# Optimization experiments

Measured on AMD Instinct MI355X. Metric: run time of the kernel, lower is better.

## Reference

```python
import jax, jax.numpy as jnp
import numpy as np

N = 50000   # nodes
E = 800000  # edges (avg degree 16)
DIMS = [(128, 128), (128, 128), (128, 64)]  # (in, out) per SAGEConv layer
EPS_BN = 1e-5
EPS_NORM = 1e-12


def _make_layer(key, din, dout):
    k1, k2 = jax.random.split(key)
    s = 1.0 / np.sqrt(din)
    return (
        jax.random.normal(k1, (dout, din), jnp.float32) * s,  # Wl: neighbor linear
        jnp.zeros((dout,), jnp.float32),                      # bl
        jax.random.normal(k2, (dout, din), jnp.float32) * s,  # Wr: root linear (no bias in PyG)
        jnp.ones((dout,), jnp.float32),                       # bn gamma
        jnp.zeros((dout,), jnp.float32),                      # bn beta
        jnp.zeros((dout,), jnp.float32),                      # bn running mean
        jnp.ones((dout,), jnp.float32),                       # bn running var
    )


def setup_inputs() -> dict:
    key = jax.random.key(0)
    kx, ke, k0, k1, k2 = jax.random.split(key, 5)
    inp = {
        "x": jax.random.normal(kx, (N, 128), jnp.float32),
        "edge_index": jax.random.randint(ke, (2, E), 0, N, dtype=jnp.int32),
    }
    for i, (k, (din, dout)) in enumerate(zip([k0, k1, k2], DIMS)):
        Wl, bl, Wr, g, b, rm, rv = _make_layer(k, din, dout)
        inp.update({f"Wl{i}": Wl, f"bl{i}": bl, f"Wr{i}": Wr,
                    f"g{i}": g, f"b{i}": b, f"rm{i}": rm, f"rv{i}": rv})
    return inp


def _sage_conv(x, src, dst, Wl, bl, Wr):
    # mean aggregation of incoming messages: gather src features, scatter-add at dst
    agg = jax.ops.segment_sum(x[src], dst, num_segments=N)          # [N, din]
    deg = jax.ops.segment_sum(jnp.ones((src.shape[0],), x.dtype), dst, num_segments=N)
    mean = agg / jnp.maximum(deg, 1.0)[:, None]
    return mean @ Wl.T + bl + x @ Wr.T


def _bn_eval(x, g, b, rm, rv):
    return g * (x - rm) * jax.lax.rsqrt(rv + EPS_BN) + b


def reference(x, edge_index,
              Wl0, bl0, Wr0, g0, b0, rm0, rv0,
              Wl1, bl1, Wr1, g1, b1, rm1, rv1,
              Wl2, bl2, Wr2, g2, b2, rm2, rv2):
    src, dst = edge_index[0], edge_index[1]
    layers = [
        (Wl0, bl0, Wr0, g0, b0, rm0, rv0),
        (Wl1, bl1, Wr1, g1, b1, rm1, rv1),
        (Wl2, bl2, Wr2, g2, b2, rm2, rv2),
    ]
    h = x
    for i, (Wl, bl, Wr, g, b, rm, rv) in enumerate(layers):
        h = _bn_eval(_sage_conv(h, src, dst, Wl, bl, Wr), g, b, rm, rv)
        if i < len(layers) - 1:
            h = jax.nn.relu(h)  # dropout is identity in eval mode
    # F.normalize(p=2, dim=1)
    return h / jnp.maximum(jnp.linalg.norm(h, axis=1, keepdims=True), EPS_NORM)
```

## Files before the change

### kernel.cpp

```cpp
#include <hip/hip_runtime.h>
#include <hip/hip_bf16.h>

#define CDIV(a,b) (((a)+(b)-1)/(b))
#define NBUCK_MAX 512
#define AGG_CAP  1536
#define AGGF_CAP 3072

typedef __attribute__((ext_vector_type(8))) short short8;
typedef __attribute__((ext_vector_type(4))) float f32x4;
typedef __attribute__((ext_vector_type(2))) float f32x2;

static __device__ __forceinline__ unsigned short f2bf(float f){
  union { float f; unsigned u; } v; v.f = f;
  unsigned r = v.u + 0x7fffu + ((v.u >> 16) & 1u);
  return (unsigned short)(r >> 16);
}
static __device__ __forceinline__ unsigned pack2(float lo, float hi){
  return (unsigned)f2bf(lo) | ((unsigned)f2bf(hi) << 16);
}
static __device__ __forceinline__ float bf2f(unsigned short s){
  union { unsigned u; float f; } v; v.u = ((unsigned)s) << 16; return v.f;
}
static __device__ __forceinline__ unsigned pk_fp8x4(float a, float b, float c, float d){
  int v = __builtin_amdgcn_cvt_pk_fp8_f32(a, b, 0, false);
  v = __builtin_amdgcn_cvt_pk_fp8_f32(c, d, v, true);
  return (unsigned)v;
}

#define ACCP16(v) { b0 += __builtin_amdgcn_cvt_pk_f32_fp8((int)v.x, false); \
                    b1 += __builtin_amdgcn_cvt_pk_f32_fp8((int)v.x, true);  \
                    b2 += __builtin_amdgcn_cvt_pk_f32_fp8((int)v.y, false); \
                    b3 += __builtin_amdgcn_cvt_pk_f32_fp8((int)v.y, true);  \
                    b4 += __builtin_amdgcn_cvt_pk_f32_fp8((int)v.z, false); \
                    b5 += __builtin_amdgcn_cvt_pk_f32_fp8((int)v.z, true);  \
                    b6 += __builtin_amdgcn_cvt_pk_f32_fp8((int)v.w, false); \
                    b7 += __builtin_amdgcn_cvt_pk_f32_fp8((int)v.w, true); }


struct WtpArgs {
  const float *W0, *W1, *bl, *g, *b, *rm, *rv;
  unsigned short* Bpk; float *sc; float *sh;
  int kblk, dout, do_bn, nblk, perm;
};

static __device__ __forceinline__ void wtp_one(const WtpArgs& a, int idx){
  int NB16 = a.kblk*32*a.dout;
  if (idx < NB16){
    int j = idx & 7, lane = (idx >> 3) & 63, rest = idx >> 9;
    int NT = a.dout >> 4;
    int nt = rest % NT, kk = rest / NT;
    int nn = nt*16 + (lane & 15);
    int k  = kk*32 + ((lane >> 4) * 8) + j;
    float v;
    if (k < 128){
      int kc = a.perm ? (((k & 7) << 4) | (k >> 3)) : k;
      v = a.W0[nn*128 + kc];
    } else {
      v = a.W1[nn*128 + (k - 128)];
    }
    a.Bpk[idx] = f2bf(v);
  } else if (a.do_bn && idx < NB16 + a.dout){
    int jj = idx - NB16;
    float s = a.g[jj] * rsqrtf(a.rv[jj] + 1e-5f);
    a.sc[jj] = s;
    a.sh[jj] = (a.bl[jj] - a.rm[jj]) * s + a.b[jj];
  }
}


__global__ __launch_bounds__(256) void k_prep(const float* __restrict__ x, int n4, unsigned* __restrict__ xb,
                                              unsigned* __restrict__ xq,
                                              const int* __restrict__ dst, int E,
                                              int* __restrict__ bcnt, int nbuck,
                                              int castBlocks, int histBlocks,
                                              WtpArgs a0, WtpArgs a1, WtpArgs a2, WtpArgs a3){
  __shared__ int s[NBUCK_MAX];
  int b = blockIdx.x, t = threadIdx.x;
  if (b < castBlocks){
    int i = b*256 + t;
    if (i < n4){
      float4 v = ((const float4*)x)[i];
      uint2 o; o.x = pack2(v.x, v.y); o.y = pack2(v.z, v.w);
      ((uint2*)xb)[i] = o;
      xq[i] = pk_fp8x4(v.x, v.y, v.z, v.w);
    }
    return;
  }
  b -= castBlocks;
  if (b < histBlocks){
    for (int i=t;i<nbuck;i+=256) s[i] = 0;
    __syncthreads();
    constexpr int EPT = 16;
    int e0 = b*256*EPT;
    #pragma unroll
    for (int i=0;i<EPT;i++){
      int e = e0 + i*256 + t;
      if (e < E) atomicAdd(&s[dst[e] >> 7], 1);
    }
    __syncthreads();
    for (int i=t;i<nbuck;i+=256){
      int c = s[i];
      if (c > 0) atomicAdd(&bcnt[i], c);
    }
    return;
  }
  b -= histBlocks;
  if (b < a0.nblk){ wtp_one(a0, b*256 + t); return; }
  b -= a0.nblk;
  if (b < a1.nblk){ wtp_one(a1, b*256 + t); return; }
  b -= a1.nblk;
  if (b < a2.nblk){ wtp_one(a2, b*256 + t); return; }
  b -= a2.nblk;
  wtp_one(a3, b*256 + t);
}

__global__ __launch_bounds__(256) void k_bucketA(const int* __restrict__ src, const int* __restrict__ dst,
                                                 int E, const int* __restrict__ bcnt,
                                                 int* __restrict__ bcur, unsigned* __restrict__ ebuf, int nbuck){
  __shared__ int scnt[NBUCK_MAX];
  __shared__ int sbase[NBUCK_MAX];
  __shared__ int sboff[NBUCK_MAX];
  __shared__ int ss[256];
  int t = threadIdx.x;
  {
    int a0 = (2*t   < nbuck) ? bcnt[2*t]   : 0;
    int a1 = (2*t+1 < nbuck) ? bcnt[2*t+1] : 0;
    ss[t] = a0 + a1; __syncthreads();
    for (int d=1; d<256; d<<=1){
      int u = (t>=d) ? ss[t-d] : 0;
      __syncthreads();
      ss[t] += u;
      __syncthreads();
    }
    int excl = ss[t] - (a0 + a1);
    if (2*t   < nbuck) sboff[2*t]   = excl;
    if (2*t+1 < nbuck) sboff[2*t+1] = excl + a0;
  }
  for (int i=t;i<nbuck;i+=256) scnt[i] = 0;
  __syncthreads();
  constexpr int EPT = 16;
  int e0 = blockIdx.x*256*EPT;
  int b[EPT]; unsigned pk[EPT];
  #pragma unroll
  for (int i=0;i<EPT;i++){
    int e = e0 + i*256 + t;
    if (e < E){
      int d = dst[e];
      b[i] = d >> 7;
      pk[i] = ((unsigned)(d & 127) << 16) | (unsigned)src[e];
      atomicAdd(&scnt[b[i]], 1);
    } else b[i] = -1;
  }
  __syncthreads();
  for (int i=t;i<nbuck;i+=256){
    int c = scnt[i];
    sbase[i] = (c > 0) ? atomicAdd(&bcur[i], c) : 0;
    scnt[i] = 0;
  }
  __syncthreads();
  #pragma unroll
  for (int i=0;i<EPT;i++){
    if (b[i] >= 0){
      int p = atomicAdd(&scnt[b[i]], 1);
      ebuf[(size_t)sboff[b[i]] + sbase[b[i]] + p] = pk[i];
    }
  }
}

__global__ __launch_bounds__(256) void k_bucketB(const unsigned* __restrict__ ebuf, const int* __restrict__ bcnt,
                                                 int nbuck, int E, int N,
                                                 int* __restrict__ offR, int* __restrict__ csr,
                                                 int* __restrict__ nodemap){
  __shared__ int sEx[NBUCK_MAX];
  __shared__ int ss[256];
  __shared__ int sdeg[128];
  __shared__ int sabs[129];
  __shared__ int cur[128];
  __shared__ unsigned skey[128];
  __shared__ int rof[128];
  int b = blockIdx.x, t = threadIdx.x;
  {
    int a0 = (2*t   < nbuck) ? bcnt[2*t]   : 0;
    int a1 = (2*t+1 < nbuck) ? bcnt[2*t+1] : 0;
    ss[t] = a0 + a1; __syncthreads();
    for (int d=1; d<256; d<<=1){
      int u = (t>=d) ? ss[t-d] : 0;
      __syncthreads();
      ss[t] += u;
      __syncthreads();
    }
    int excl = ss[t] - (a0 + a1);
    if (2*t   < nbuck) sEx[2*t]   = excl;
    if (2*t+1 < nbuck) sEx[2*t+1] = excl + a0;
  }
  if (t < 128){ sdeg[t] = 0; cur[t] = 0; }
  __syncthreads();
  int e0 = sEx[b];
  int e1 = (b+1 < nbuck) ? sEx[b+1] : E;
  for (int e = e0 + t; e < e1; e += 256)
    atomicAdd(&sdeg[ebuf[e] >> 16], 1);
  __syncthreads();
  if (t < 128) skey[t] = ((unsigned)sdeg[t] << 7) | (unsigned)(127 - t);
  __syncthreads();
  #pragma unroll
  for (int k=2; k<=128; k<<=1){
    #pragma unroll
    for (int j=k>>1; j>0; j>>=1){
      if (t < 128){
        int p = t ^ j;
        if (p > t){
          unsigned x = skey[t], y = skey[p];
          bool swap = ((t & k) == 0) ? (x < y) : (x > y);
          if (swap){ skey[t] = y; skey[p] = x; }
        }
      }
      __syncthreads();
    }
  }
  if (t < 128){
    int lid = 127 - (int)(skey[t] & 127u);
    rof[lid] = t;
    sdeg[t] = (int)(skey[t] >> 7);
  }
  __syncthreads();
  for (int d=1; d<128; d<<=1){
    int u = (t < 128 && t >= d) ? sdeg[t-d] : 0;
    __syncthreads();
    if (t < 128) sdeg[t] += u;
    __syncthreads();
  }
  if (t == 0) sabs[0] = e0;
  if (t < 128) sabs[t+1] = e0 + sdeg[t];
  __syncthreads();
  int n0 = b << 7, n1 = min(n0 + 128, N);
  int cnt = n1 - n0;
  if (t <= cnt) offR[n0 + t] = sabs[t];
  if (t < cnt)  nodemap[n0 + t] = n0 + (127 - (int)(skey[t] & 127u));
  for (int e = e0 + t; e < e1; e += 256){
    unsigned pr = ebuf[e];
    int ln = (int)(pr >> 16);
    int p = atomicAdd(&cur[ln], 1);
    csr[sabs[rof[ln]] + p] = (int)(pr & 0xffffu);
  }
}


__global__ __launch_bounds__(256) void k_agg(const uint4* __restrict__ hq4, const int* __restrict__ offR,
                                             const int* __restrict__ csr, const int* __restrict__ nodemap,
                                             int n, uint4* __restrict__ mean4){
  __shared__ int scsr[AGG_CAP];
  __shared__ int sw[2];
  int t = threadIdx.x;
  int nodeblk = blockIdx.x * 32;
  if (t < 2) sw[t] = offR[min(nodeblk + t*32, n)];
  __syncthreads();
  int e0b = sw[0];
  int span = sw[1] - e0b;
  for (int i = t; i < span && i < AGG_CAP; i += 256) scsr[i] = csr[e0b + i];
  __syncthreads();

  int lane = t & 63;
  int sl = lane & 7;
  int idx = nodeblk + (t >> 3);
  bool valid = idx < n;
  int s0 = valid ? offR[idx]   : 0;
  int s1 = valid ? offR[idx+1] : 0;
  int node = valid ? nodemap[idx] : 0;
  f32x2 b0={0,0},b1={0,0},b2={0,0},b3={0,0},b4={0,0},b5={0,0},b6={0,0},b7={0,0};
  int e = s0;
  for (; e + 8 <= s1; e += 8){
    int le = e - e0b;
    int i0,i1,i2,i3,i4,i5,i6,i7;
    if (le + 8 <= AGG_CAP){
      i0 = scsr[le];   i1 = scsr[le+1]; i2 = scsr[le+2]; i3 = scsr[le+3];
      i4 = scsr[le+4]; i5 = scsr[le+5]; i6 = scsr[le+6]; i7 = scsr[le+7];
    } else {
      i0 = csr[e];   i1 = csr[e+1]; i2 = csr[e+2]; i3 = csr[e+3];
      i4 = csr[e+4]; i5 = csr[e+5]; i6 = csr[e+6]; i7 = csr[e+7];
    }
    uint4 v0 = hq4[(size_t)i0*8 + sl];
    uint4 v1 = hq4[(size_t)i1*8 + sl];
    uint4 v2 = hq4[(size_t)i2*8 + sl];
    uint4 v3 = hq4[(size_t)i3*8 + sl];
    uint4 v4 = hq4[(size_t)i4*8 + sl];
    uint4 v5 = hq4[(size_t)i5*8 + sl];
    uint4 v6 = hq4[(size_t)i6*8 + sl];
    uint4 v7 = hq4[(size_t)i7*8 + sl];
    ACCP16(v0); ACCP16(v1); ACCP16(v2); ACCP16(v3);
    ACCP16(v4); ACCP16(v5); ACCP16(v6); ACCP16(v7);
  }
  for (; e + 4 <= s1; e += 4){
    int le = e - e0b;
    int i0,i1,i2,i3;
    if (le + 4 <= AGG_CAP){
      i0 = scsr[le]; i1 = scsr[le+1]; i2 = scsr[le+2]; i3 = scsr[le+3];
    } else {
      i0 = csr[e]; i1 = csr[e+1]; i2 = csr[e+2]; i3 = csr[e+3];
    }
    uint4 v0 = hq4[(size_t)i0*8 + sl];
    uint4 v1 = hq4[(size_t)i1*8 + sl];
    uint4 v2 = hq4[(size_t)i2*8 + sl];
    uint4 v3 = hq4[(size_t)i3*8 + sl];
    ACCP16(v0); ACCP16(v1); ACCP16(v2); ACCP16(v3);
  }
  for (; e < s1; e++){
    int le = e - e0b;
    int ii = (le < AGG_CAP) ? scsr[le] : csr[e];
    uint4 v = hq4[(size_t)ii*8 + sl];
    ACCP16(v);
  }
  if (valid){
    int d = s1 - s0;
    float inv = 1.0f / (float)(d > 0 ? d : 1);
    uint4 o0, o1;
    o0.x = pack2(b0.x*inv, b0.y*inv);  o0.y = pack2(b1.x*inv, b1.y*inv);
    o0.z = pack2(b2.x*inv, b2.y*inv);  o0.w = pack2(b3.x*inv, b3.y*inv);
    o1.x = pack2(b4.x*inv, b4.y*inv);  o1.y = pack2(b5.x*inv, b5.y*inv);
    o1.z = pack2(b6.x*inv, b6.y*inv);  o1.w = pack2(b7.x*inv, b7.y*inv);
    size_t base = (size_t)node*16 + (size_t)sl*2;
    mean4[base]   = o0;
    mean4[base+1] = o1;
  }
}


template<bool YL>
__global__ __launch_bounds__(256, 2) void k_gemm_hid(
    const unsigned short* __restrict__ A0, const unsigned short* __restrict__ A1,
    const unsigned short* __restrict__ Bpk, const float* __restrict__ sc,
    const float* __restrict__ sh, const unsigned short* __restrict__ BpkL,
    unsigned short* __restrict__ outh, unsigned* __restrict__ outq,
    unsigned* __restrict__ outyl, int n){
  __shared__ unsigned short Bs[256*128];
  int t = threadIdx.x;
  {
    const uint4* s = (const uint4*)Bpk;
    uint4* d = (uint4*)Bs;
    #pragma unroll
    for (int i=0;i<16;i++) d[i*256 + t] = s[i*256 + t];
  }
  __syncthreads();

  int lane = t & 63, w = t >> 6;
  int quad = lane >> 4, c = lane & 15;
  int mb = blockIdx.x*128, woff = w*32;
  int r0 = mb + woff + c;
  int r1 = r0 + 16;

  f32x4 acc[2][8];
  #pragma unroll
  for (int mt=0;mt<2;mt++)
    #pragma unroll
    for (int nt=0;nt<8;nt++) acc[mt][nt] = (f32x4){0.f,0.f,0.f,0.f};

  #pragma unroll
  for (int kk=0; kk<8; kk++){
    const unsigned short* ab = (kk >= 4) ? A1 : A0;
    int ka = (kk & 3)*32 + quad*8;
    short8 a0 = {0,0,0,0,0,0,0,0}, a1 = {0,0,0,0,0,0,0,0};
    if (r0 < n) a0 = *(const short8*)(ab + (size_t)r0*128 + ka);
    if (r1 < n) a1 = *(const short8*)(ab + (size_t)r1*128 + ka);
    #pragma unroll
    for (int nt=0; nt<8; nt++){
      short8 b = *(const short8*)&Bs[(size_t)((kk*8 + nt)*64 + lane)*8];
      acc[0][nt] = __builtin_amdgcn_mfma_f32_16x16x32_bf16(a0, b, acc[0][nt], 0, 0, 0);
      acc[1][nt] = __builtin_amdgcn_mfma_f32_16x16x32_bf16(a1, b, acc[1][nt], 0, 0, 0);
    }
  }

  float scv[8], shv[8];
  #pragma unroll
  for (int nt=0;nt<8;nt++){ scv[nt] = sc[nt*16 + c]; shv[nt] = sh[nt*16 + c]; }

  #pragma unroll
  for (int mt=0; mt<2; mt++){
    #pragma unroll
    for (int r=0;r<4;r++){
      int row = mb + woff + mt*16 + quad*4 + r;
      if (row < n){
        float u[8];
        #pragma unroll
        for (int nt=0;nt<8;nt++){
          float uu = acc[mt][nt][r]*scv[nt] + shv[nt];
          u[nt] = fmaxf(uu, 0.f);
          outh[(size_t)row*128 + nt*16 + c] = f2bf(u[nt]);
        }
        if constexpr (!YL){
          uint2 q;
          q.x = pk_fp8x4(u[0], u[1], u[2], u[3]);
          q.y = pk_fp8x4(u[4], u[5], u[6], u[7]);
          ((uint2*)outq)[(size_t)row*16 + c] = q;
        }
      }
    }
  }

  if constexpr (YL){
    __syncthreads();
    {
      uint4* d = (uint4*)Bs;
      const uint4* s4 = (const uint4*)outh;
      #pragma unroll
      for (int i=0;i<8;i++){
        int idx = i*256 + t;
        int row = idx >> 4;
        int gr = mb + row; if (gr > n-1) gr = n-1;
        d[idx] = s4[(size_t)gr*16 + (idx & 15)];
      }
      const uint4* sL = (const uint4*)BpkL;
      #pragma unroll
      for (int i=0;i<4;i++) d[2048 + i*256 + t] = sL[i*256 + t];
    }
    __syncthreads();
    f32x4 acc2[2][4];
    #pragma unroll
    for (int mt=0;mt<2;mt++)
      #pragma unroll
      for (int nt=0;nt<4;nt++) acc2[mt][nt] = (f32x4){0.f,0.f,0.f,0.f};
    int r0l = woff + c, r1l = r0l + 16;
    #pragma unroll
    for (int kk=0; kk<4; kk++){
      int ka = kk*32 + quad*8;
      short8 a0 = *(const short8*)&Bs[(size_t)r0l*128 + ka];
      short8 a1 = *(const short8*)&Bs[(size_t)r1l*128 + ka];
      #pragma unroll
      for (int nt=0; nt<4; nt++){
        short8 b = *(const short8*)&Bs[16384 + (size_t)((kk*4 + nt)*64 + lane)*8];
        acc2[0][nt] = __builtin_amdgcn_mfma_f32_16x16x32_bf16(a0, b, acc2[0][nt], 0, 0, 0);
        acc2[1][nt] = __builtin_amdgcn_mfma_f32_16x16x32_bf16(a1, b, acc2[1][nt], 0, 0, 0);
      }
    }
    #pragma unroll
    for (int mt=0; mt<2; mt++){
      #pragma unroll
      for (int r=0;r<4;r++){
        int row = mb + woff + mt*16 + quad*4 + r;
        if (row < n){
          unsigned q = pk_fp8x4(acc2[0][0][r], acc2[0][1][r], acc2[0][2][r], acc2[0][3][r]);
          unsigned q1 = pk_fp8x4(acc2[1][0][r], acc2[1][1][r], acc2[1][2][r], acc2[1][3][r]);
          outyl[(size_t)row*16 + c] = (mt == 0) ? q : q1;
        }
      }
    }
  }
}


__global__ __launch_bounds__(256, 2) void k_aggf(
    const uint4* __restrict__ ylq4, const int* __restrict__ offR, const int* __restrict__ csr,
    const int* __restrict__ nodemap,
    const unsigned short* __restrict__ A0, const unsigned short* __restrict__ BpkR,
    const float* __restrict__ sc, const float* __restrict__ sh,
    float* __restrict__ outf, int n){
  __shared__ unsigned short Ms[128*64];
  __shared__ unsigned short Bs[128*64];
  __shared__ int scsr[AGGF_CAP];
  __shared__ int sw[2];
  int t = threadIdx.x;
  int mb = blockIdx.x*128;
  if (t < 2) sw[t] = offR[min(mb + t*128, n)];
  {
    const uint4* s = (const uint4*)BpkR;
    uint4* d = (uint4*)Bs;
    #pragma unroll
    for (int i=0;i<4;i++) d[i*256 + t] = s[i*256 + t];
  }
  __syncthreads();
  int e0b = sw[0];
  int span = sw[1] - e0b;
  for (int i = t; i < span && i < AGGF_CAP; i += 256) scsr[i] = csr[e0b + i];
  __syncthreads();

  int lane = t & 63, w = t >> 6;
  int sl4 = lane & 3;

  #pragma unroll
  for (int it=0; it<2; it++){
    int rk = w*32 + it*16 + (lane >> 2);
    int idx = mb + rk;
    bool valid = idx < n;
    int s0 = valid ? offR[idx]   : 0;
    int s1 = valid ? offR[idx+1] : 0;
    int ln = valid ? (nodemap[idx] - mb) : rk;
    f32x2 b0={0,0},b1={0,0},b2={0,0},b3={0,0},b4={0,0},b5={0,0},b6={0,0},b7={0,0};
    int e = s0;
    for (; e + 8 <= s1; e += 8){
      int le = e - e0b;
      int i0,i1,i2,i3,i4,i5,i6,i7;
      if (le + 8 <= AGGF_CAP){
        i0 = scsr[le];   i1 = scsr[le+1]; i2 = scsr[le+2]; i3 = scsr[le+3];
        i4 = scsr[le+4]; i5 = scsr[le+5]; i6 = scsr[le+6]; i7 = scsr[le+7];
      } else {
        i0 = csr[e];   i1 = csr[e+1]; i2 = csr[e+2]; i3 = csr[e+3];
        i4 = csr[e+4]; i5 = csr[e+5]; i6 = csr[e+6]; i7 = csr[e+7];
      }
      uint4 v0 = ylq4[(size_t)i0*4 + sl4];
      uint4 v1 = ylq4[(size_t)i1*4 + sl4];
      uint4 v2 = ylq4[(size_t)i2*4 + sl4];
      uint4 v3 = ylq4[(size_t)i3*4 + sl4];
      uint4 v4 = ylq4[(size_t)i4*4 + sl4];
      uint4 v5 = ylq4[(size_t)i5*4 + sl4];
      uint4 v6 = ylq4[(size_t)i6*4 + sl4];
      uint4 v7 = ylq4[(size_t)i7*4 + sl4];
      ACCP16(v0); ACCP16(v1); ACCP16(v2); ACCP16(v3);
      ACCP16(v4); ACCP16(v5); ACCP16(v6); ACCP16(v7);
    }
    for (; e + 4 <= s1; e += 4){
      int le = e - e0b;
      int i0,i1,i2,i3;
      if (le + 4 <= AGGF_CAP){
        i0 = scsr[le]; i1 = scsr[le+1]; i2 = scsr[le+2]; i3 = scsr[le+3];
      } else {
        i0 = csr[e]; i1 = csr[e+1]; i2 = csr[e+2]; i3 = csr[e+3];
      }
      uint4 v0 = ylq4[(size_t)i0*4 + sl4];
      uint4 v1 = ylq4[(size_t)i1*4 + sl4];
      uint4 v2 = ylq4[(size_t)i2*4 + sl4];
      uint4 v3 = ylq4[(size_t)i3*4 + sl4];
      ACCP16(v0); ACCP16(v1); ACCP16(v2); ACCP16(v3);
    }
    for (; e < s1; e++){
      int le = e - e0b;
      int ii = (le < AGGF_CAP) ? scsr[le] : csr[e];
      uint4 v = ylq4[(size_t)ii*4 + sl4];
      ACCP16(v);
    }
    int d = s1 - s0;
    float inv = 1.0f / (float)(d > 0 ? d : 1);
    uint4 o0, o1;
    o0.x = pack2(b0.x*inv, b0.y*inv);  o0.y = pack2(b1.x*inv, b1.y*inv);
    o0.z = pack2(b2.x*inv, b2.y*inv);  o0.w = pack2(b3.x*inv, b3.y*inv);
    o1.x = pack2(b4.x*inv, b4.y*inv);  o1.y = pack2(b5.x*inv, b5.y*inv);
    o1.z = pack2(b6.x*inv, b6.y*inv);  o1.w = pack2(b7.x*inv, b7.y*inv);
    ((uint4*)Ms)[ln*8 + sl4*2]     = o0;
    ((uint4*)Ms)[ln*8 + sl4*2 + 1] = o1;
  }
  __syncthreads();

  int quad = lane >> 4, c = lane & 15;
  int woff = w*32;
  int r0 = mb + woff + c;
  int r1 = r0 + 16;
  f32x4 acc[2][4];
  #pragma unroll
  for (int mt=0;mt<2;mt++)
    #pragma unroll
    for (int nt=0;nt<4;nt++) acc[mt][nt] = (f32x4){0.f,0.f,0.f,0.f};
  #pragma unroll
  for (int kk=0; kk<4; kk++){
    int ka = kk*32 + quad*8;
    short8 a0 = {0,0,0,0,0,0,0,0}, a1 = {0,0,0,0,0,0,0,0};
    if (r0 < n) a0 = *(const short8*)(A0 + (size_t)r0*128 + ka);
    if (r1 < n) a1 = *(const short8*)(A0 + (size_t)r1*128 + ka);
    #pragma unroll
    for (int nt=0; nt<4; nt++){
      short8 b = *(const short8*)&Bs[(size_t)((kk*4 + nt)*64 + lane)*8];
      acc[0][nt] = __builtin_amdgcn_mfma_f32_16x16x32_bf16(a0, b, acc[0][nt], 0, 0, 0);
      acc[1][nt] = __builtin_amdgcn_mfma_f32_16x16x32_bf16(a1, b, acc[1][nt], 0, 0, 0);
    }
  }

  float scv[4], shv[4];
  #pragma unroll
  for (int nt=0;nt<4;nt++){ scv[nt] = sc[nt*16 + c]; shv[nt] = sh[nt*16 + c]; }

  #pragma unroll
  for (int mt=0; mt<2; mt++){
    #pragma unroll
    for (int r=0;r<4;r++){
      int lr = woff + mt*16 + quad*4 + r;
      int row = mb + lr;
      float v[4];
      float ss = 0.f;
      if (row < n){
        #pragma unroll
        for (int nt=0;nt<4;nt++){
          float u = acc[mt][nt][r] + bf2f(Ms[lr*64 + c*4 + nt]);
          u = u*scv[nt] + shv[nt];
          v[nt] = u;
          ss += u*u;
        }
      } else {
        #pragma unroll
        for (int nt=0;nt<4;nt++) v[nt] = 0.f;
      }
      ss += __shfl_xor(ss, 1, 64);
      ss += __shfl_xor(ss, 2, 64);
      ss += __shfl_xor(ss, 4, 64);
      ss += __shfl_xor(ss, 8, 64);
      float rn = 1.0f / fmaxf(sqrtf(ss), 1e-12f);
      if (row < n){
        #pragma unroll
        for (int nt=0;nt<4;nt++) outf[(size_t)row*64 + nt*16 + c] = v[nt]*rn;
      }
    }
  }
}


extern "C" void kernel_launch(void* const* d_in, const int* in_sizes, int n_in,
                              void* d_out, int out_size, void* d_ws, size_t ws_size,
                              hipStream_t stream){
  const float* x = (const float*)d_in[0];
  const int* ei  = (const int*)d_in[1];
  int N = in_sizes[0] / 128;
  int E = in_sizes[1] / 2;
  const int* esrc = ei;
  const int* edst = ei + E;
  int nbuck = CDIV(N, 128);

  const float *Wl[3], *bl[3], *Wr[3], *g[3], *bb[3], *rm[3], *rv[3];
  int dout[3];
  for (int i=0;i<3;i++){
    int base = 2 + 7*i;
    Wl[i]=(const float*)d_in[base];   bl[i]=(const float*)d_in[base+1];
    Wr[i]=(const float*)d_in[base+2]; g[i] =(const float*)d_in[base+3];
    bb[i]=(const float*)d_in[base+4]; rm[i]=(const float*)d_in[base+5];
    rv[i]=(const float*)d_in[base+6];
    dout[i] = in_sizes[base] / 128;
  }

  char* p = (char*)d_ws;
  size_t o = 0;
  auto alloc = [&](size_t bytes)->void*{ void* r = p + o; o += (bytes + 255) & ~(size_t)255; return r; };
  int* bz    = (int*)alloc((size_t)2*nbuck*4);
  int* bcnt  = bz;
  int* bcur  = bz + nbuck;
  int* offR  = (int*)alloc((size_t)(N+1)*4);
  int* nodemap = (int*)alloc((size_t)N*4);
  int* csr   = (int*)alloc((size_t)E*4);
  unsigned* ebuf = (unsigned*)alloc((size_t)E*4);
  unsigned* xb   = (unsigned*)alloc((size_t)N*64*4);
  unsigned* xq   = (unsigned*)alloc((size_t)N*128);
  unsigned* mb   = (unsigned*)alloc((size_t)N*64*4);
  unsigned* h_a  = (unsigned*)alloc((size_t)N*64*4);
  unsigned* haq  = (unsigned*)alloc((size_t)N*128);
  unsigned* h_b  = (unsigned*)alloc((size_t)N*64*4);
  unsigned* ylb  = (unsigned*)alloc((size_t)N*64);
  unsigned short* Bpk01[2];
  float* sc[3]; float* sh[3];
  for (int i=0;i<2;i++) Bpk01[i] = (unsigned short*)alloc((size_t)256*dout[i]*2);
  unsigned short* BpkL = (unsigned short*)alloc((size_t)128*dout[2]*2);
  unsigned short* BpkR = (unsigned short*)alloc((size_t)128*dout[2]*2);
  for (int i=0;i<3;i++){
    sc[i] = (float*)alloc((size_t)dout[i]*4);
    sh[i] = (float*)alloc((size_t)dout[i]*4);
  }

  hipMemsetAsync(bz, 0, (size_t)2*nbuck*4, stream);

  WtpArgs wa[4];
  wa[0] = { Wl[0], Wr[0], bl[0], g[0], bb[0], rm[0], rv[0], Bpk01[0], sc[0], sh[0], 8, dout[0], 1, CDIV(256*dout[0]+dout[0],256), 0 };
  wa[1] = { Wl[1], Wr[1], bl[1], g[1], bb[1], rm[1], rv[1], Bpk01[1], sc[1], sh[1], 8, dout[1], 1, CDIV(256*dout[1]+dout[1],256), 1 };
  wa[2] = { Wl[2], nullptr, nullptr, nullptr, nullptr, nullptr, nullptr, BpkL, nullptr, nullptr, 4, dout[2], 0, CDIV(128*dout[2],256), 0 };
  wa[3] = { Wr[2], nullptr, bl[2], g[2], bb[2], rm[2], rv[2], BpkR, sc[2], sh[2], 4, dout[2], 1, CDIV(128*dout[2]+dout[2],256), 0 };

  int castBlocks = CDIV(N*32, 256);
  int histBlocks = CDIV(E, 256*16);
  int prepBlocks = castBlocks + histBlocks + wa[0].nblk + wa[1].nblk + wa[2].nblk + wa[3].nblk;
  k_prep   <<<prepBlocks,256,0,stream>>>(x, N*32, xb, xq, edst, E, bcnt, nbuck, castBlocks, histBlocks,
                                         wa[0], wa[1], wa[2], wa[3]);
  k_bucketA<<<CDIV(E,256*16),256,0,stream>>>(esrc, edst, E, bcnt, bcur, ebuf, nbuck);
  k_bucketB<<<nbuck,256,0,stream>>>(ebuf, bcnt, nbuck, E, N, offR, csr, nodemap);

  k_agg<<<CDIV(N,32),256,0,stream>>>((const uint4*)xq, offR, csr, nodemap, N, (uint4*)mb);
  k_gemm_hid<false><<<CDIV(N,128),256,0,stream>>>((const unsigned short*)mb, (const unsigned short*)xb,
                                                  Bpk01[0], sc[0], sh[0], nullptr,
                                                  (unsigned short*)h_a, haq, nullptr, N);
  k_agg<<<CDIV(N,32),256,0,stream>>>((const uint4*)haq, offR, csr, nodemap, N, (uint4*)mb);
  k_gemm_hid<true><<<CDIV(N,128),256,0,stream>>>((const unsigned short*)mb, (const unsigned short*)h_a,
                                                 Bpk01[1], sc[1], sh[1], BpkL,
                                                 (unsigned short*)h_b, nullptr, ylb, N);
  k_aggf<<<CDIV(N,128),256,0,stream>>>((const uint4*)ylb, offR, csr, nodemap,
                                       (const unsigned short*)h_b, BpkR, sc[2], sh[2],
                                       (float*)d_out, N);
}
```

Before: 239.1 us.

## Fuse mean aggregation into hidden-layer GEMM kernels via shared-memory tile

Merges the separate aggregation and hidden GEMM kernels so each 128-node block gathers neighbor means into a padded shared-memory tile and feeds it straight into the MFMA loop. This drops the global mean buffer round-trip and two launches, and in the YL variant keeps the hidden output in shared memory for the second projection instead of re-reading it from global. The GEMM B operand is now read from global/cache instead of staged in LDS, and aggregation parallelism per block drops (128 nodes per block), which may reduce latency hiding for the gather.

Result: no change. 242.8 us (+1.5%).

```diff
diff --git a/kernel.cpp b/kernel.cpp
--- a/kernel.cpp
+++ b/kernel.cpp
@@ -3,7 +3,7 @@
 
 #define CDIV(a,b) (((a)+(b)-1)/(b))
 #define NBUCK_MAX 512
-#define AGG_CAP  1536
+#define FUSE_CAP 4096
 #define AGGF_CAP 3072
 
 typedef __attribute__((ext_vector_type(8))) short short8;
@@ -245,71 +245,83 @@
 }
 
 
-__global__ __launch_bounds__(256) void k_agg(const uint4* __restrict__ hq4, const int* __restrict__ offR,
-                                             const int* __restrict__ csr, const int* __restrict__ nodemap,
-                                             int n, uint4* __restrict__ mean4){
-  __shared__ int scsr[AGG_CAP];
+template<bool YL>
+__global__ __launch_bounds__(256, 2) void k_fuse(
+    const uint4* __restrict__ hq4, const int* __restrict__ offR, const int* __restrict__ csr,
+    const int* __restrict__ nodemap,
+    const unsigned short* __restrict__ Ag, const unsigned short* __restrict__ Bpk,
+    const float* __restrict__ sc, const float* __restrict__ sh,
+    const unsigned short* __restrict__ BpkL,
+    unsigned short* __restrict__ outh, unsigned* __restrict__ outq,
+    unsigned* __restrict__ outyl, int n){
+  __shared__ uint4 Ms4[128*17];
+  __shared__ uint4 sBL4[1024];
   __shared__ int sw[2];
+  unsigned short* Ms = (unsigned short*)Ms4;
+  int* scsr = (int*)sBL4;
   int t = threadIdx.x;
-  int nodeblk = blockIdx.x * 32;
-  if (t < 2) sw[t] = offR[min(nodeblk + t*32, n)];
+  int mb = blockIdx.x*128;
+  if (t < 2) sw[t] = offR[min(mb + t*128, n)];
   __syncthreads();
   int e0b = sw[0];
   int span = sw[1] - e0b;
-  for (int i = t; i < span && i < AGG_CAP; i += 256) scsr[i] = csr[e0b + i];
-  __syncthreads();
-
-  int lane = t & 63;
+  for (int i = t; i < span && i < FUSE_CAP; i += 256) scsr[i] = csr[e0b + i];
+  __syncthreads();
+
+  int lane = t & 63, w = t >> 6;
   int sl = lane & 7;
-  int idx = nodeblk + (t >> 3);
-  bool valid = idx < n;
-  int s0 = valid ? offR[idx]   : 0;
-  int s1 = valid ? offR[idx+1] : 0;
-  int node = valid ? nodemap[idx] : 0;
-  f32x2 b0={0,0},b1={0,0},b2={0,0},b3={0,0},b4={0,0},b5={0,0},b6={0,0},b7={0,0};
-  int e = s0;
-  for (; e + 8 <= s1; e += 8){
-    int le = e - e0b;
-    int i0,i1,i2,i3,i4,i5,i6,i7;
-    if (le + 8 <= AGG_CAP){
-      i0 = scsr[le];   i1 = scsr[le+1]; i2 = scsr[le+2]; i3 = scsr[le+3];
-      i4 = scsr[le+4]; i5 = scsr[le+5]; i6 = scsr[le+6]; i7 = scsr[le+7];
-    } else {
-      i0 = csr[e];   i1 = csr[e+1]; i2 = csr[e+2]; i3 = csr[e+3];
-      i4 = csr[e+4]; i5 = csr[e+5]; i6 = csr[e+6]; i7 = csr[e+7];
-    }
-    uint4 v0 = hq4[(size_t)i0*8 + sl];
-    uint4 v1 = hq4[(size_t)i1*8 + sl];
-    uint4 v2 = hq4[(size_t)i2*8 + sl];
-    uint4 v3 = hq4[(size_t)i3*8 + sl];
-    uint4 v4 = hq4[(size_t)i4*8 + sl];
-    uint4 v5 = hq4[(size_t)i5*8 + sl];
-    uint4 v6 = hq4[(size_t)i6*8 + sl];
-    uint4 v7 = hq4[(size_t)i7*8 + sl];
-    ACCP16(v0); ACCP16(v1); ACCP16(v2); ACCP16(v3);
-    ACCP16(v4); ACCP16(v5); ACCP16(v6); ACCP16(v7);
-  }
-  for (; e + 4 <= s1; e += 4){
-    int le = e - e0b;
-    int i0,i1,i2,i3;
-    if (le + 4 <= AGG_CAP){
-      i0 = scsr[le]; i1 = scsr[le+1]; i2 = scsr[le+2]; i3 = scsr[le+3];
-    } else {
-      i0 = csr[e]; i1 = csr[e+1]; i2 = csr[e+2]; i3 = csr[e+3];
-    }
-    uint4 v0 = hq4[(size_t)i0*8 + sl];
-    uint4 v1 = hq4[(size_t)i1*8 + sl];
-    uint4 v2 = hq4[(size_t)i2*8 + sl];
-    uint4 v3 = hq4[(size_t)i3*8 + sl];
-    ACCP16(v0); ACCP16(v1); ACCP16(v2); ACCP16(v3);
-  }
-  for (; e < s1; e++){
-    int le = e - e0b;
-    int ii = (le < AGG_CAP) ? scsr[le] : csr[e];
-    uint4 v = hq4[(size_t)ii*8 + sl];
-    ACCP16(v);
-  }
-  if (valid){
+
+  #pragma unroll
+  for (int it=0; it<4; it++){
+    int rk = w*32 + it*8 + (lane >> 3);
+    int idx = mb + rk;
+    bool valid = idx < n;
+    int s0 = valid ? offR[idx]   : 0;
+    int s1 = valid ? offR[idx+1] : 0;
+    int ln = valid ? (nodemap[idx] - mb) : rk;
+    f32x2 b0={0,0},b1={0,0},b2={0,0},b3={0,0},b4={0,0},b5={0,0},b6={0,0},b7={0,0};
+    int e = s0;
+    for (; e + 8 <= s1; e += 8){
+      int le = e - e0b;
+      int i0,i1,i2,i3,i4,i5,i6,i7;
+      if (le + 8 <= FUSE_CAP){
+        i0 = scsr[le];   i1 = scsr[le+1]; i2 = scsr[le+2]; i3 = scsr[le+3];
+        i4 = scsr[le+4]; i5 = scsr[le+5]; i6 = scsr[le+6]; i7 = scsr[le+7];
+      } else {
+        i0 = csr[e];   i1 = csr[e+1]; i2 = csr[e+2]; i3 = csr[e+3];
+        i4 = csr[e+4]; i5 = csr[e+5]; i6 = csr[e+6]; i7 = csr[e+7];
+      }
+      uint4 v0 = hq4[(size_t)i0*8 + sl];
+      uint4 v1 = hq4[(size_t)i1*8 + sl];
+      uint4 v2 = hq4[(size_t)i2*8 + sl];
+      uint4 v3 = hq4[(size_t)i3*8 + sl];
+      uint4 v4 = hq4[(size_t)i4*8 + sl];
+      uint4 v5 = hq4[(size_t)i5*8 + sl];
+      uint4 v6 = hq4[(size_t)i6*8 + sl];
+      uint4 v7 = hq4[(size_t)i7*8 + sl];
+      ACCP16(v0); ACCP16(v1); ACCP16(v2); ACCP16(v3);
+      ACCP16(v4); ACCP16(v5); ACCP16(v6); ACCP16(v7);
+    }
+    for (; e + 4 <= s1; e += 4){
+      int le = e - e0b;
+      int i0,i1,i2,i3;
+      if (le + 4 <= FUSE_CAP){
+        i0 = scsr[le]; i1 = scsr[le+1]; i2 = scsr[le+2]; i3 = scsr[le+3];
+      } else {
+        i0 = csr[e]; i1 = csr[e+1]; i2 = csr[e+2]; i3 = csr[e+3];
+      }
+      uint4 v0 = hq4[(size_t)i0*8 + sl];
+      uint4 v1 = hq4[(size_t)i1*8 + sl];
+      uint4 v2 = hq4[(size_t)i2*8 + sl];
+      uint4 v3 = hq4[(size_t)i3*8 + sl];
+      ACCP16(v0); ACCP16(v1); ACCP16(v2); ACCP16(v3);
+    }
+    for (; e < s1; e++){
+      int le = e - e0b;
+      int ii = (le < FUSE_CAP) ? scsr[le] : csr[e];
+      uint4 v = hq4[(size_t)ii*8 + sl];
+      ACCP16(v);
+    }
     int d = s1 - s0;
     float inv = 1.0f / (float)(d > 0 ? d : 1);
     uint4 o0, o1;
@@ -317,33 +329,13 @@
     o0.z = pack2(b2.x*inv, b2.y*inv);  o0.w = pack2(b3.x*inv, b3.y*inv);
     o1.x = pack2(b4.x*inv, b4.y*inv);  o1.y = pack2(b5.x*inv, b5.y*inv);
     o1.z = pack2(b6.x*inv, b6.y*inv);  o1.w = pack2(b7.x*inv, b7.y*inv);
-    size_t base = (size_t)node*16 + (size_t)sl*2;
-    mean4[base]   = o0;
-    mean4[base+1] = o1;
-  }
-}
-
-
-template<bool YL>
-__global__ __launch_bounds__(256, 2) void k_gemm_hid(
-    const unsigned short* __restrict__ A0, const unsigned short* __restrict__ A1,
-    const unsigned short* __restrict__ Bpk, const float* __restrict__ sc,
-    const float* __restrict__ sh, const unsigned short* __restrict__ BpkL,
-    unsigned short* __restrict__ outh, unsigned* __restrict__ outq,
-    unsigned* __restrict__ outyl, int n){
-  __shared__ unsigned short Bs[256*128];
-  int t = threadIdx.x;
-  {
-    const uint4* s = (const uint4*)Bpk;
-    uint4* d = (uint4*)Bs;
-    #pragma unroll
-    for (int i=0;i<16;i++) d[i*256 + t] = s[i*256 + t];
-  }
-  __syncthreads();
-
-  int lane = t & 63, w = t >> 6;
+    Ms4[ln*17 + sl*2]     = o0;
+    Ms4[ln*17 + sl*2 + 1] = o1;
+  }
+  __syncthreads();
+
   int quad = lane >> 4, c = lane & 15;
-  int mb = blockIdx.x*128, woff = w*32;
+  int woff = w*32;
   int r0 = mb + woff + c;
   int r1 = r0 + 16;
 
@@ -355,14 +347,19 @@
 
   #pragma unroll
   for (int kk=0; kk<8; kk++){
-    const unsigned short* ab = (kk >= 4) ? A1 : A0;
     int ka = (kk & 3)*32 + quad*8;
-    short8 a0 = {0,0,0,0,0,0,0,0}, a1 = {0,0,0,0,0,0,0,0};
-    if (r0 < n) a0 = *(const short8*)(ab + (size_t)r0*128 + ka);
-    if (r1 < n) a1 = *(const short8*)(ab + (size_t)r1*128 + ka);
+    short8 a0, a1;
+    if (kk < 4){
+      a0 = *(const short8*)&Ms[(woff + c)*136 + ka];
+      a1 = *(const short8*)&Ms[(woff + c + 16)*136 + ka];
+    } else {
+      a0 = (short8){0,0,0,0,0,0,0,0}; a1 = (short8){0,0,0,0,0,0,0,0};
+      if (r0 < n) a0 = *(const short8*)(Ag + (size_t)r0*128 + ka);
+      if (r1 < n) a1 = *(const short8*)(Ag + (size_t)r1*128 + ka);
+    }
     #pragma unroll
     for (int nt=0; nt<8; nt++){
-      short8 b = *(const short8*)&Bs[(size_t)((kk*8 + nt)*64 + lane)*8];
+      short8 b = *(const short8*)(Bpk + (size_t)((kk*8 + nt)*64 + lane)*8);
       acc[0][nt] = __builtin_amdgcn_mfma_f32_16x16x32_bf16(a0, b, acc[0][nt], 0, 0, 0);
       acc[1][nt] = __builtin_amdgcn_mfma_f32_16x16x32_bf16(a1, b, acc[1][nt], 0, 0, 0);
     }
@@ -372,11 +369,14 @@
   #pragma unroll
   for (int nt=0;nt<8;nt++){ scv[nt] = sc[nt*16 + c]; shv[nt] = sh[nt*16 + c]; }
 
+  if constexpr (YL) __syncthreads();
+
   #pragma unroll
   for (int mt=0; mt<2; mt++){
     #pragma unroll
     for (int r=0;r<4;r++){
-      int row = mb + woff + mt*16 + quad*4 + r;
+      int lrow = woff + mt*16 + quad*4 + r;
+      int row = mb + lrow;
       if (row < n){
         float u[8];
         #pragma unroll
@@ -390,28 +390,25 @@
           q.x = pk_fp8x4(u[0], u[1], u[2], u[3]);
           q.y = pk_fp8x4(u[4], u[5], u[6], u[7]);
           ((uint2*)outq)[(size_t)row*16 + c] = q;
+        } else {
+          #pragma unroll
+          for (int nt=0;nt<8;nt++) Ms[lrow*136 + nt*16 + c] = f2bf(u[nt]);
         }
+      } else if constexpr (YL) {
+        #pragma unroll
+        for (int nt=0;nt<8;nt++) Ms[lrow*136 + nt*16 + c] = 0;
       }
     }
   }
 
   if constexpr (YL){
-    __syncthreads();
     {
-      uint4* d = (uint4*)Bs;
-      const uint4* s4 = (const uint4*)outh;
-      #pragma unroll
-      for (int i=0;i<8;i++){
-        int idx = i*256 + t;
-        int row = idx >> 4;
-        int gr = mb + row; if (gr > n-1) gr = n-1;
-        d[idx] = s4[(size_t)gr*16 + (idx & 15)];
-      }
       const uint4* sL = (const uint4*)BpkL;
       #pragma unroll
-      for (int i=0;i<4;i++) d[2048 + i*256 + t] = sL[i*256 + t];
+      for (int i=0;i<4;i++) sBL4[i*256 + t] = sL[i*256 + t];
     }
     __syncthreads();
+    unsigned short* BsL = (unsigned short*)sBL4;
     f32x4 acc2[2][4];
     #pragma unroll
     for (int mt=0;mt<2;mt++)
@@ -421,11 +418,11 @@
     #pragma unroll
     for (int kk=0; kk<4; kk++){
       int ka = kk*32 + quad*8;
-      short8 a0 = *(const short8*)&Bs[(size_t)r0l*128 + ka];
-      short8 a1 = *(const short8*)&Bs[(size_t)r1l*128 + ka];
+      short8 a0 = *(const short8*)&Ms[r0l*136 + ka];
+      short8 a1 = *(const short8*)&Ms[r1l*136 + ka];
       #pragma unroll
       for (int nt=0; nt<4; nt++){
-        short8 b = *(const short8*)&Bs[16384 + (size_t)((kk*4 + nt)*64 + lane)*8];
+        short8 b = *(const short8*)&BsL[(size_t)((kk*4 + nt)*64 + lane)*8];
         acc2[0][nt] = __builtin_amdgcn_mfma_f32_16x16x32_bf16(a0, b, acc2[0][nt], 0, 0, 0);
         acc2[1][nt] = __builtin_amdgcn_mfma_f32_16x16x32_bf16(a1, b, acc2[1][nt], 0, 0, 0);
       }
@@ -436,7 +433,7 @@
       for (int r=0;r<4;r++){
         int row = mb + woff + mt*16 + quad*4 + r;
         if (row < n){
-          unsigned q = pk_fp8x4(acc2[0][0][r], acc2[0][1][r], acc2[0][2][r], acc2[0][3][r]);
+          unsigned q  = pk_fp8x4(acc2[0][0][r], acc2[0][1][r], acc2[0][2][r], acc2[0][3][r]);
           unsigned q1 = pk_fp8x4(acc2[1][0][r], acc2[1][1][r], acc2[1][2][r], acc2[1][3][r]);
           outyl[(size_t)row*16 + c] = (mt == 0) ? q : q1;
         }
@@ -632,7 +629,6 @@
   unsigned* ebuf = (unsigned*)alloc((size_t)E*4);
   unsigned* xb   = (unsigned*)alloc((size_t)N*64*4);
   unsigned* xq   = (unsigned*)alloc((size_t)N*128);
-  unsigned* mb   = (unsigned*)alloc((size_t)N*64*4);
   unsigned* h_a  = (unsigned*)alloc((size_t)N*64*4);
   unsigned* haq  = (unsigned*)alloc((size_t)N*128);
   unsigned* h_b  = (unsigned*)alloc((size_t)N*64*4);
@@ -663,15 +659,13 @@
   k_bucketA<<<CDIV(E,256*16),256,0,stream>>>(esrc, edst, E, bcnt, bcur, ebuf, nbuck);
   k_bucketB<<<nbuck,256,0,stream>>>(ebuf, bcnt, nbuck, E, N, offR, csr, nodemap);
 
-  k_agg<<<CDIV(N,32),256,0,stream>>>((const uint4*)xq, offR, csr, nodemap, N, (uint4*)mb);
-  k_gemm_hid<false><<<CDIV(N,128),256,0,stream>>>((const unsigned short*)mb, (const unsigned short*)xb,
-                                                  Bpk01[0], sc[0], sh[0], nullptr,
-                                                  (unsigned short*)h_a, haq, nullptr, N);
-  k_agg<<<CDIV(N,32),256,0,stream>>>((const uint4*)haq, offR, csr, nodemap, N, (uint4*)mb);
-  k_gemm_hid<true><<<CDIV(N,128),256,0,stream>>>((const unsigned short*)mb, (const unsigned short*)h_a,
-                                                 Bpk01[1], sc[1], sh[1], BpkL,
-                                                 (unsigned short*)h_b, nullptr, ylb, N);
-  k_aggf<<<CDIV(N,128),256,0,stream>>>((const uint4*)ylb, offR, csr, nodemap,
-                                       (const unsigned short*)h_b, BpkR, sc[2], sh[2],
-                                       (float*)d_out, N);
-}
+  k_fuse<false><<<nbuck,256,0,stream>>>((const uint4*)xq, offR, csr, nodemap,
+                                        (const unsigned short*)xb, Bpk01[0], sc[0], sh[0], nullptr,
+                                        (unsigned short*)h_a, haq, nullptr, N);
+  k_fuse<true><<<nbuck,256,0,stream>>>((const uint4*)haq, offR, csr, nodemap,
+                                       (const unsigned short*)h_a, Bpk01[1], sc[1], sh[1], BpkL,
+                                       (unsigned short*)h_b, nullptr, ylb, N);
+  k_aggf<<<nbuck,256,0,stream>>>((const uint4*)ylb, offR, csr, nodemap,
+                                 (const unsigned short*)h_b, BpkR, sc[2], sh[2],
+                                 (float*)d_out, N);
+}
```
